# Performance work log

Hardware: AMD Instinct MI355X
Metric: run time of the kernel (lower is better)

Reference implementation:

```python
import jax, jax.numpy as jnp
import numpy as np

IN_SIZE = 64
OUT_SIZE = 64
H1 = 2
H2 = 2
BATCH = 8192


def setup_inputs() -> dict:
    key = jax.random.key(0)
    ks = jax.random.split(key, 8)
    x = jax.random.normal(ks[0], (BATCH, IN_SIZE), dtype=jnp.float32)
    # Per-connection tiny MLP params; grid of (In, Out) subnets.
    # Layer 1: Linear(1, H1) -> w1:[In,Out,H1], b1:[In,Out,H1]
    # Layer 2: Linear(H1, H2) -> w2:[In,Out,H2,H1], b2:[In,Out,H2]
    # Layer 3: Linear(H2, 1) -> w3:[In,Out,H2], b3:[In,Out]
    s1 = 1.0  # kaiming-ish scale for fan_in=1
    s2 = 1.0 / np.sqrt(H1)
    s3 = 1.0 / np.sqrt(H2)
    w1 = jax.random.uniform(ks[1], (IN_SIZE, OUT_SIZE, H1), jnp.float32, -s1, s1)
    b1 = jax.random.uniform(ks[2], (IN_SIZE, OUT_SIZE, H1), jnp.float32, -s1, s1)
    w2 = jax.random.uniform(ks[3], (IN_SIZE, OUT_SIZE, H2, H1), jnp.float32, -s2, s2)
    b2 = jax.random.uniform(ks[4], (IN_SIZE, OUT_SIZE, H2), jnp.float32, -s2, s2)
    w3 = jax.random.uniform(ks[5], (IN_SIZE, OUT_SIZE, H2), jnp.float32, -s3, s3)
    b3 = jax.random.uniform(ks[6], (IN_SIZE, OUT_SIZE), jnp.float32, -s3, s3)
    return {"x": x, "w1": w1, "b1": b1, "w2": w2, "b2": b2, "w3": w3, "b3": b3}


def reference(x, w1, b1, w2, b2, w3, b3):
    # x: [B, In]. Each (in, out) connection has its own tiny 3-layer MLP on a scalar.
    # h1: [B, In, Out, H1] = relu(x * w1 + b1)  (input dim is 1, so it's a scale)
    h1 = jax.nn.relu(x[:, :, None, None] * w1[None] + b1[None])
    # h2: [B, In, Out, H2]
    h2 = jax.nn.relu(jnp.einsum('bioh,iokh->biok', h1, w2) + b2[None])
    # scalar output per connection: [B, In, Out]
    y = jnp.einsum('biok,iok->bio', h2, w3) + b3[None]
    # KAN combination: sum contributions over inputs -> [B, Out]
    return jnp.sum(y, axis=1)
```

## Files before the change

kernel.cpp:

```cpp
#include <hip/hip_runtime.h>


#define IN_SIZE  64
#define OUT_SIZE 64
#define BATCH    8192

constexpr int I_CHUNK = 8;
constexpr int WAVES   = 8;
constexpr int BT      = 16;
constexpr int PAD     = 9;

__device__ __forceinline__ void conn(float xv, float2 W1, float2 B1,
                                     float4 W2, float2 B2, float2 W3,
                                     float& s) {
    const float h0 = fmaxf(fmaf(xv, W1.x, B1.x), 0.f);
    const float h1 = fmaxf(fmaf(xv, W1.y, B1.y), 0.f);
    float u0 = fmaf(h1, W2.y, fmaf(h0, W2.x, B2.x));
    float u1 = fmaf(h1, W2.w, fmaf(h0, W2.z, B2.y));
    u0 = fmaxf(u0, 0.f);
    u1 = fmaxf(u1, 0.f);
    s = fmaf(u0, W3.x, s);
    s = fmaf(u1, W3.y, s);
}

__global__ __launch_bounds__(512, 4) void kan_kernel(
    const float* __restrict__ x,
    const float* __restrict__ w1, const float* __restrict__ b1,
    const float* __restrict__ w2, const float* __restrict__ b2,
    const float* __restrict__ w3, const float* __restrict__ b3,
    float* __restrict__ out)
{
    const int tid   = threadIdx.x;
    const int o     = tid & 63;
    const int wv    = tid >> 6;
    const int brow0 = blockIdx.x * BT;

    __shared__ float xs[BT * IN_SIZE];
    __shared__ float ps[BT * OUT_SIZE * PAD];

    {
        const float2* xg = reinterpret_cast<const float2*>(x + brow0 * IN_SIZE);
        reinterpret_cast<float2*>(xs)[tid] = xg[tid];
    }

    const int i0 = wv * I_CHUNK;
    float2 W1[I_CHUNK], B1[I_CHUNK], B2[I_CHUNK], W3[I_CHUNK];
    float4 W2[I_CHUNK];
    float bacc = 0.f;
    #pragma unroll
    for (int ic = 0; ic < I_CHUNK; ++ic) {
        const int base = (i0 + ic) * OUT_SIZE + o;
        W1[ic] = reinterpret_cast<const float2*>(w1)[base];
        B1[ic] = reinterpret_cast<const float2*>(b1)[base];
        W2[ic] = reinterpret_cast<const float4*>(w2)[base];
        B2[ic] = reinterpret_cast<const float2*>(b2)[base];
        W3[ic] = reinterpret_cast<const float2*>(w3)[base];
        bacc  += b3[base];
    }

    __syncthreads();

    #pragma unroll
    for (int r = 0; r < BT; ++r) {
        const float4 xa = *reinterpret_cast<const float4*>(xs + r * IN_SIZE + i0);
        const float4 xb = *reinterpret_cast<const float4*>(xs + r * IN_SIZE + i0 + 4);
        float s = bacc;
        conn(xa.x, W1[0], B1[0], W2[0], B2[0], W3[0], s);
        conn(xa.y, W1[1], B1[1], W2[1], B2[1], W3[1], s);
        conn(xa.z, W1[2], B1[2], W2[2], B2[2], W3[2], s);
        conn(xa.w, W1[3], B1[3], W2[3], B2[3], W3[3], s);
        conn(xb.x, W1[4], B1[4], W2[4], B2[4], W3[4], s);
        conn(xb.y, W1[5], B1[5], W2[5], B2[5], W3[5], s);
        conn(xb.z, W1[6], B1[6], W2[6], B2[6], W3[6], s);
        conn(xb.w, W1[7], B1[7], W2[7], B2[7], W3[7], s);
        ps[(r * OUT_SIZE + o) * PAD + wv] = s;
    }

    __syncthreads();

    #pragma unroll
    for (int t = tid; t < BT * OUT_SIZE; t += 512) {
        const float* p = ps + t * PAD;
        const float v = ((p[0] + p[1]) + (p[2] + p[3]))
                      + ((p[4] + p[5]) + (p[6] + p[7]));
        out[brow0 * OUT_SIZE + t] = v;
    }
}

extern "C" void kernel_launch(void* const* d_in, const int* in_sizes, int n_in,
                              void* d_out, int out_size, void* d_ws, size_t ws_size,
                              hipStream_t stream) {
    const float* x  = (const float*)d_in[0];
    const float* w1 = (const float*)d_in[1];
    const float* b1 = (const float*)d_in[2];
    const float* w2 = (const float*)d_in[3];
    const float* b2 = (const float*)d_in[4];
    const float* w3 = (const float*)d_in[5];
    const float* b3 = (const float*)d_in[6];
    float* out = (float*)d_out;

    const int grid = BATCH / BT;
    kan_kernel<<<grid, 512, 0, stream>>>(x, w1, b1, w2, b2, w3, b3, out);
}
```

Before: 18.00 us.

## Split inputs across 16 waves and reduce row groups incrementally in 1024-thread blocks

Blocks grow to 1024 threads with 16 waves, each owning 4 inputs, and each block now covers 32 batch rows. The cross-wave partial sums are reduced in groups of 8 rows through a smaller shared buffer, with a barrier before and after each group. Empty asm constraints pin the per-connection weights in registers. The aim is to halve the number of blocks, and with it the redundant weight loads per block, while shrinking shared memory. The cost is more barriers and only one large block per CU.

```diff
diff --git a/kernel.cpp b/kernel.cpp
--- a/kernel.cpp
+++ b/kernel.cpp
@@ -5,10 +5,15 @@
 #define OUT_SIZE 64
 #define BATCH    8192
 
-constexpr int I_CHUNK = 8;
-constexpr int WAVES   = 8;
-constexpr int BT      = 16;
-constexpr int PAD     = 9;
+constexpr int WAVES   = 16;
+constexpr int I_CHUNK = 4;
+constexpr int BT      = 32;
+constexpr int RG      = 8;
+constexpr int PAD     = 17;
+
+__device__ __forceinline__ void pin(float& v) {
+    asm volatile("" : "+v"(v));
+}
 
 __device__ __forceinline__ void conn(float xv, float2 W1, float2 B1,
                                      float4 W2, float2 B2, float2 W3,
@@ -23,7 +28,7 @@
     s = fmaf(u1, W3.y, s);
 }
 
-__global__ __launch_bounds__(512, 4) void kan_kernel(
+__global__ __launch_bounds__(1024, 4) void kan_kernel(
     const float* __restrict__ x,
     const float* __restrict__ w1, const float* __restrict__ b1,
     const float* __restrict__ w2, const float* __restrict__ b2,
@@ -36,7 +41,7 @@
     const int brow0 = blockIdx.x * BT;
 
     __shared__ float xs[BT * IN_SIZE];
-    __shared__ float ps[BT * OUT_SIZE * PAD];
+    __shared__ float ps[RG * OUT_SIZE * PAD];
 
     {
         const float2* xg = reinterpret_cast<const float2*>(x + brow0 * IN_SIZE);
@@ -57,33 +62,39 @@
         W3[ic] = reinterpret_cast<const float2*>(w3)[base];
         bacc  += b3[base];
     }
-
-    __syncthreads();
-
     #pragma unroll
-    for (int r = 0; r < BT; ++r) {
-        const float4 xa = *reinterpret_cast<const float4*>(xs + r * IN_SIZE + i0);
-        const float4 xb = *reinterpret_cast<const float4*>(xs + r * IN_SIZE + i0 + 4);
-        float s = bacc;
-        conn(xa.x, W1[0], B1[0], W2[0], B2[0], W3[0], s);
-        conn(xa.y, W1[1], B1[1], W2[1], B2[1], W3[1], s);
-        conn(xa.z, W1[2], B1[2], W2[2], B2[2], W3[2], s);
-        conn(xa.w, W1[3], B1[3], W2[3], B2[3], W3[3], s);
-        conn(xb.x, W1[4], B1[4], W2[4], B2[4], W3[4], s);
-        conn(xb.y, W1[5], B1[5], W2[5], B2[5], W3[5], s);
-        conn(xb.z, W1[6], B1[6], W2[6], B2[6], W3[6], s);
-        conn(xb.w, W1[7], B1[7], W2[7], B2[7], W3[7], s);
-        ps[(r * OUT_SIZE + o) * PAD + wv] = s;
+    for (int ic = 0; ic < I_CHUNK; ++ic) {
+        pin(W1[ic].x); pin(W1[ic].y);  pin(B1[ic].x); pin(B1[ic].y);
+        pin(W2[ic].x); pin(W2[ic].y);  pin(W2[ic].z); pin(W2[ic].w);
+        pin(B2[ic].x); pin(B2[ic].y);  pin(W3[ic].x); pin(W3[ic].y);
     }
 
     __syncthreads();
 
     #pragma unroll
-    for (int t = tid; t < BT * OUT_SIZE; t += 512) {
-        const float* p = ps + t * PAD;
-        const float v = ((p[0] + p[1]) + (p[2] + p[3]))
-                      + ((p[4] + p[5]) + (p[6] + p[7]));
-        out[brow0 * OUT_SIZE + t] = v;
+    for (int g = 0; g < BT / RG; ++g) {
+        #pragma unroll
+        for (int rr = 0; rr < RG; ++rr) {
+            const int r = g * RG + rr;
+            const float4 xa = *reinterpret_cast<const float4*>(xs + r * IN_SIZE + i0);
+            float s = bacc;
+            conn(xa.x, W1[0], B1[0], W2[0], B2[0], W3[0], s);
+            conn(xa.y, W1[1], B1[1], W2[1], B2[1], W3[1], s);
+            conn(xa.z, W1[2], B1[2], W2[2], B2[2], W3[2], s);
+            conn(xa.w, W1[3], B1[3], W2[3], B2[3], W3[3], s);
+            ps[(rr * OUT_SIZE + o) * PAD + wv] = s;
+        }
+        __syncthreads();
+
+        if (tid < RG * OUT_SIZE) {
+            const float* p = ps + tid * PAD;
+            const float v = (((p[0]  + p[1])  + (p[2]  + p[3]))
+                          +  ((p[4]  + p[5])  + (p[6]  + p[7])))
+                          + (((p[8]  + p[9])  + (p[10] + p[11]))
+                          +  ((p[12] + p[13]) + (p[14] + p[15])));
+            out[(brow0 + g * RG) * OUT_SIZE + tid] = v;
+        }
+        __syncthreads();
     }
 }
 
@@ -100,5 +111,5 @@
     float* out = (float*)d_out;
 
     const int grid = BATCH / BT;
-    kan_kernel<<<grid, 512, 0, stream>>>(x, w1, b1, w2, b2, w3, b3, out);
+    kan_kernel<<<grid, 1024, 0, stream>>>(x, w1, b1, w2, b2, w3, b3, out);
 }
```

Result: faster. 17.11 us (-5.0%).
